# Performance work log

Measured on AMD Instinct MI355X. Metric: run time of the kernel, lower is better.

## Reference

```python
import jax, jax.numpy as jnp
import numpy as np

DIM = 768
TIME_DIM = 768
NUM_HEADS = 12
NUM_PATCHES = 784
GRID = 28  # sqrt(NUM_PATCHES)
REL_MAX = 2 * GRID - 1  # 55


def _rel_pos_indices():
    # Faithful to the torch buffer: relative_position_index = (dh + g-1) + (dw + g-1)
    coords = np.stack(np.meshgrid(np.arange(GRID), np.arange(GRID), indexing='ij'))  # [2,g,g]
    cf = coords.reshape(2, -1)  # [2,N]
    rel = cf[:, :, None] - cf[:, None, :]  # [2,N,N]
    rel = rel.transpose(1, 2, 0)
    rel[:, :, 0] += GRID - 1
    rel[:, :, 1] += GRID - 1
    idx = rel.sum(-1)  # [N,N], values in [0, 2*(2g-2)]
    # forward then splits this summed index (as written in the source):
    ih = idx // REL_MAX
    iw = idx % REL_MAX
    return jnp.asarray(ih, jnp.int32), jnp.asarray(iw, jnp.int32)


def setup_inputs() -> dict:
    key = jax.random.key(0)
    ks = jax.random.split(key, 16)
    B = 8
    s = 0.02
    inp = {
        'x_s': jax.random.normal(ks[0], (B, NUM_PATCHES, DIM), jnp.float32),
        'x_t': jax.random.normal(ks[1], (B, TIME_DIM), jnp.float32),
        'Wqs': jax.random.normal(ks[2], (DIM, DIM), jnp.float32) * s,
        'Wqt': jax.random.normal(ks[3], (TIME_DIM, DIM), jnp.float32) * s,
        'Wks': jax.random.normal(ks[4], (DIM, DIM), jnp.float32) * s,
        'Wkt': jax.random.normal(ks[5], (TIME_DIM, DIM), jnp.float32) * s,
        'Wvs': jax.random.normal(ks[6], (DIM, DIM), jnp.float32) * s,
        'Wvt': jax.random.normal(ks[7], (TIME_DIM, DIM), jnp.float32) * s,
        'rpb_table': jax.random.normal(ks[8], (REL_MAX, REL_MAX, NUM_HEADS), jnp.float32) * s,
        'proj_w': jax.random.normal(ks[9], (DIM, DIM), jnp.float32) * s,
        'proj_b': jnp.zeros((DIM,), jnp.float32),
    }
    return inp


def reference(x_s, x_t, Wqs, Wqt, Wks, Wkt, Wvs, Wvt, rpb_table, proj_w, proj_b):
    B, N, D = x_s.shape
    H = NUM_HEADS
    hd = D // H
    scale = hd ** -0.5

    # time-embed fused QKV: q = x_s @ Wqs + x_t @ Wqt (broadcast over tokens)
    q = x_s @ Wqs + (x_t @ Wqt)[:, None, :]
    k = x_s @ Wks + (x_t @ Wkt)[:, None, :]
    v = x_s @ Wvs + (x_t @ Wvt)[:, None, :]

    q = q.reshape(B, N, H, hd).transpose(0, 2, 1, 3)  # [B,H,N,hd]
    k = k.reshape(B, N, H, hd).transpose(0, 2, 1, 3)
    v = v.reshape(B, N, H, hd).transpose(0, 2, 1, 3)

    attn = jnp.einsum('bhnd,bhmd->bhnm', q, k) * scale  # [B,H,N,N]

    ih, iw = _rel_pos_indices()  # [N,N] each
    bias = rpb_table[ih, iw]  # [N,N,H]
    attn = attn + bias.transpose(2, 0, 1)[None]  # [1,H,N,N]

    attn = jax.nn.softmax(attn, axis=-1)
    x = jnp.einsum('bhnm,bhmd->bhnd', attn, v)
    x = x.transpose(0, 2, 1, 3).reshape(B, N, D)
    return x @ proj_w + proj_b
```

## Files before the change

kernel.cpp:

```cpp
#include <hip/hip_runtime.h>
#include <stdint.h>

#define DIM 768
#define NP  784
#define NH  12
#define HD  64
#define BATCH 8
#define MROWS (BATCH*NP)
#define MPAD 832
#define NCHUNK 32
#define KCH 24

using bf16x8 = __attribute__((ext_vector_type(8))) short;
using bf16x4 = __attribute__((ext_vector_type(4))) short;
using f32x4  = __attribute__((ext_vector_type(4))) float;

__device__ __forceinline__ short f2bf(float f) {
  union { float f; uint32_t u; } c; c.f = f;
  uint32_t u = c.u;
  u += 0x7FFFu + ((u >> 16) & 1u);
  return (short)(u >> 16);
}

__device__ __forceinline__ void gld_lds16(const void* g, void* l) {
  __builtin_amdgcn_global_load_lds((const __attribute__((address_space(1))) uint32_t*)g,
                                   (__attribute__((address_space(3))) uint32_t*)l,
                                   16, 0, 0);
}

__global__ __launch_bounds__(256) void cvt_bf16_kernel(const float* __restrict__ src,
                                                       short* __restrict__ dst, int n8) {
  int i = blockIdx.x * 256 + threadIdx.x;
  if (i >= n8) return;
  const float4* s = (const float4*)src;
  float4 a = s[2*i], b = s[2*i+1];
  bf16x8 o;
  o[0]=f2bf(a.x); o[1]=f2bf(a.y); o[2]=f2bf(a.z); o[3]=f2bf(a.w);
  o[4]=f2bf(b.x); o[5]=f2bf(b.y); o[6]=f2bf(b.z); o[7]=f2bf(b.w);
  ((bf16x8*)dst)[i] = o;
}

__global__ __launch_bounds__(256) void wtrans_kernel(const float* __restrict__ w0,
                                                     const float* __restrict__ w1,
                                                     const float* __restrict__ w2,
                                                     const float* __restrict__ w3,
                                                     short* __restrict__ dst) {
  __shared__ float tile[32][33];
  const int z = blockIdx.z;
  const float* src = (z==0) ? w0 : (z==1) ? w1 : (z==2) ? w2 : w3;
  short* d = dst + (size_t)z * DIM * DIM;
  const int n0 = blockIdx.x*32, k0 = blockIdx.y*32;
  const int tx = threadIdx.x, ty = threadIdx.y;
#pragma unroll
  for (int i=0;i<4;i++) tile[ty+i*8][tx] = src[(size_t)(k0+ty+i*8)*DIM + n0+tx];
  __syncthreads();
#pragma unroll
  for (int i=0;i<4;i++) d[(size_t)(n0+ty+i*8)*DIM + k0+tx] = f2bf(tile[tx][ty+i*8]);
}

__global__ __launch_bounds__(256) void tvec1_kernel(const float* __restrict__ x_t,
                                                    const float* __restrict__ wq,
                                                    const float* __restrict__ wk,
                                                    const float* __restrict__ wv,
                                                    float* __restrict__ part) {
  const int z = blockIdx.x, kc = blockIdx.y;
  const float* w = (z==0) ? wq : (z==1) ? wk : wv;
  const int d = threadIdx.x;
  __shared__ float xs[BATCH][KCH];
  if (threadIdx.x < BATCH*KCH)
    xs[threadIdx.x / KCH][threadIdx.x % KCH] =
        x_t[(size_t)(threadIdx.x / KCH)*DIM + kc*KCH + threadIdx.x % KCH];
  __syncthreads();
  float a0[BATCH] = {}, a1[BATCH] = {}, a2[BATCH] = {};
#pragma unroll 4
  for (int k = 0; k < KCH; ++k) {
    const float* wr = w + (size_t)(kc*KCH + k)*DIM + d;
    float w0 = wr[0], w1 = wr[256], w2 = wr[512];
#pragma unroll
    for (int b = 0; b < BATCH; ++b) {
      float xv = xs[b][k];
      a0[b] += xv*w0; a1[b] += xv*w1; a2[b] += xv*w2;
    }
  }
#pragma unroll
  for (int b = 0; b < BATCH; ++b) {
    float* p = part + (((size_t)z*NCHUNK + kc)*BATCH + b)*DIM + d;
    p[0] = a0[b]; p[256] = a1[b]; p[512] = a2[b];
  }
}

__global__ __launch_bounds__(256) void tvec2_kernel(const float* __restrict__ part,
                                                    float* __restrict__ t) {
  const int i = blockIdx.x*256 + threadIdx.x;
  if (i >= 3*BATCH*DIM) return;
  const int z = i / (BATCH*DIM), rem = i % (BATCH*DIM);
  float s = 0.f;
#pragma unroll 8
  for (int c = 0; c < NCHUNK; ++c)
    s += part[((size_t)z*NCHUNK + c)*BATCH*DIM + rem];
  t[i] = s;
}

template<int MODE>
__global__ __launch_bounds__(256) void gemm_kernel(const short* __restrict__ A,
                                                   const short* __restrict__ Bw,
                                                   const float* __restrict__ aux,
                                                   short* __restrict__ outq,
                                                   short* __restrict__ outk,
                                                   short* __restrict__ outv,
                                                   float* __restrict__ outf) {
  __shared__ short As[128*32];
  __shared__ short Bs[128*32];
  const int bx = blockIdx.x, by = blockIdx.y, z = blockIdx.z;
  const short* Bz = Bw + (size_t)z * DIM * DIM;
  const int tid = threadIdx.x, w = tid>>6, lane = tid&63;
  const int wr = w>>1, wc = w&1, ln15 = lane&15, lg = lane>>4;
  const int m0 = by*128, n0 = bx*128;

  f32x4 acc[4][4] = {};

  for (int kt=0; kt<24; ++kt) {
    const int k0 = kt*32;
    __syncthreads();
#pragma unroll
    for (int i=0;i<2;i++) {
      const int inst = w*2 + i;
      const int off  = inst*1024 + lane*16;
      const int row  = off >> 6;
      const int ce   = (off & 63) >> 1;
      gld_lds16(A  + (size_t)(m0+row)*DIM + k0 + ce, (char*)As + (size_t)inst*1024);
      gld_lds16(Bz + (size_t)(n0+row)*DIM + k0 + ce, (char*)Bs + (size_t)inst*1024);
    }
    __syncthreads();
    bf16x8 af[4], bfr[4];
#pragma unroll
    for (int mi=0;mi<4;mi++) af[mi]  = *(const bf16x8*)&As[(wr*64+mi*16+ln15)*32 + lg*8];
#pragma unroll
    for (int ni=0;ni<4;ni++) bfr[ni] = *(const bf16x8*)&Bs[(wc*64+ni*16+ln15)*32 + lg*8];
#pragma unroll
    for (int mi=0;mi<4;mi++)
#pragma unroll
      for (int ni=0;ni<4;ni++)
        acc[mi][ni] = __builtin_amdgcn_mfma_f32_16x16x32_bf16(af[mi], bfr[ni], acc[mi][ni], 0,0,0);
  }

  if (MODE == 0) {
    const float scl = (z==0) ? 0.125f : 1.0f;
#pragma unroll
    for (int mi=0;mi<4;mi++) {
#pragma unroll
      for (int j=0;j<4;j++) {
        const int r  = m0 + wr*64 + mi*16 + lg*4 + j;
        const int bb = r / NP;
        const int m  = r - bb*NP;
        const float* tv = aux + ((size_t)z*BATCH + bb) * DIM;
        if (z == 0) {
#pragma unroll
          for (int ni=0;ni<4;ni++) {
            const int gcol = n0 + wc*64 + ni*16 + ln15;
            outq[(size_t)r*DIM + gcol] = f2bf((acc[mi][ni][j] + tv[gcol]) * scl);
          }
        } else if (z == 1) {
#pragma unroll
          for (int ni=0;ni<4;ni++) {
            const int gcol = n0 + wc*64 + ni*16 + ln15;
            const int h = gcol >> 6, d = gcol & 63;
            outk[((size_t)(bb*NH + h)*MPAD + m)*HD + d] = f2bf(acc[mi][ni][j] + tv[gcol]);
          }
        }
      }
      if (MODE == 0 && z == 2) {
        const int r0 = m0 + wr*64 + mi*16 + lg*4;
        const int bb = r0 / NP;
        const int m  = r0 - bb*NP;
        const float* tv = aux + ((size_t)2*BATCH + bb) * DIM;
#pragma unroll
        for (int ni=0;ni<4;ni++) {
          const int gcol = n0 + wc*64 + ni*16 + ln15;
          const int h = gcol >> 6, d = gcol & 63;
          const float tb = tv[gcol];
          bf16x4 ov;
          ov[0] = f2bf(acc[mi][ni][0] + tb);
          ov[1] = f2bf(acc[mi][ni][1] + tb);
          ov[2] = f2bf(acc[mi][ni][2] + tb);
          ov[3] = f2bf(acc[mi][ni][3] + tb);
          *(bf16x4*)&outv[((size_t)(bb*NH + h)*HD + d)*MPAD + m] = ov;
        }
      }
    }
  } else {
#pragma unroll
    for (int mi=0;mi<4;mi++)
#pragma unroll
      for (int j=0;j<4;j++) {
        const int r = m0 + wr*64 + mi*16 + lg*4 + j;
#pragma unroll
        for (int ni=0;ni<4;ni++) {
          const int gcol = n0 + wc*64 + ni*16 + ln15;
          outf[(size_t)r*DIM + gcol] = acc[mi][ni][j] + aux[gcol];
        }
      }
  }
}

__global__ __launch_bounds__(256) void attn2_kernel(const short* __restrict__ Qb,
                                                    const short* __restrict__ Kt,
                                                    const short* __restrict__ Vt,
                                                    const float* __restrict__ rpb,
                                                    short* __restrict__ Ob) {
  __shared__ short kt[2][4096];
  __shared__ short vt[2][4096];
  __shared__ float bias_ext[112];
  __shared__ short msum[MPAD];
  const int qt = blockIdx.x, h = blockIdx.y, b = blockIdx.z;
  const int q0 = qt*64, tid = threadIdx.x, w = tid >> 6, lane = tid & 63;
  const int ln15 = lane & 15, lg = lane >> 4;

  if (tid < 109) bias_ext[tid + 2] = rpb[(tid/55)*(55*NH) + (tid%55)*NH + h];
  if (tid == 109) { bias_ext[0] = 0.f; bias_ext[1] = 0.f; bias_ext[111] = 0.f; }
  for (int i = tid; i < MPAD; i += 256) msum[i] = (short)(i/28 + i%28);

  const bool active = (q0 + w*16) < NP;
  const int q_idx = q0 + w*16 + ln15;
  bf16x8 qf0 = {}, qf1 = {};
  if (active) {
    const short* qp = Qb + ((size_t)(b*NP) + q_idx)*DIM + h*HD + lg*8;
    qf0 = *(const bf16x8*)qp;
    qf1 = *(const bf16x8*)(qp + 32);
  }
  const int qs = q_idx/28 + q_idx%28;

  const int lr = lane >> 3, lc = lane & 7;
  const int swe = (lc ^ lr) << 3;
  const size_t bh = (size_t)(b*NH + h);
  const short* kp0 = Kt + (bh*MPAD + (size_t)(w*8 + lr))*HD + swe;
  const short* kp1 = kp0 + 32*HD;
  const short* vp0 = Vt + (bh*HD + (size_t)(w*8 + lr))*MPAD + swe;
  const short* vp1 = vp0 + 32*MPAD;

#define STAGE4(BUF) { \
    char* kb_ = (char*)kt[BUF]; char* vb_ = (char*)vt[BUF]; \
    gld_lds16(kp0, kb_ + w*1024); \
    gld_lds16(kp1, kb_ + (w+4)*1024); \
    gld_lds16(vp0, vb_ + w*1024); \
    gld_lds16(vp1, vb_ + (w+4)*1024); \
    kp0 += 64*HD; kp1 += 64*HD; vp0 += 64; vp1 += 64; }

  float m_run = -3.0e38f, l_run = 0.f;
  f32x4 o0 = {}, o1 = {}, o2 = {}, o3 = {};

  STAGE4(0)

  for (int t = 0; t < 13; ++t) {
    const int cur = t & 1;
    const int m0 = t * 64;
    __syncthreads();
    if (t < 12) STAGE4(cur^1)
    if (active) {
      const char* kb = (const char*)kt[cur];
      const int sw = (ln15 & 7) << 4;
      f32x4 s[4];
#pragma unroll
      for (int mc = 0; mc < 4; ++mc) {
        const int rb = (mc*16 + ln15) * 128;
        bf16x8 kf0 = *(const bf16x8*)(kb + rb + ((lg*16) ^ sw));
        bf16x8 kf1 = *(const bf16x8*)(kb + rb + ((lg*16 + 64) ^ sw));
        f32x4 acc = {};
        acc = __builtin_amdgcn_mfma_f32_16x16x32_bf16(kf0, qf0, acc, 0,0,0);
        acc = __builtin_amdgcn_mfma_f32_16x16x32_bf16(kf1, qf1, acc, 0,0,0);
        s[mc] = acc;
      }
#pragma unroll
      for (int mc = 0; mc < 4; ++mc) {
        const int mb = m0 + mc*16 + lg*4;
        bf16x4 ms4 = *(const bf16x4*)&msum[mb];
#pragma unroll
        for (int j = 0; j < 4; ++j)
          s[mc][j] += bias_ext[qs - (int)ms4[j] + 56];
      }
      if (m0 + 64 > NP) {
#pragma unroll
        for (int mc = 0; mc < 4; ++mc)
#pragma unroll
          for (int j = 0; j < 4; ++j)
            if (m0 + mc*16 + lg*4 + j >= NP) s[mc][j] = -1e30f;
      }
      float tm = s[0][0];
#pragma unroll
      for (int mc = 0; mc < 4; ++mc)
#pragma unroll
        for (int j = 0; j < 4; ++j) tm = fmaxf(tm, s[mc][j]);
      tm = fmaxf(tm, __shfl_xor(tm, 16));
      tm = fmaxf(tm, __shfl_xor(tm, 32));
      const float m_new = fmaxf(m_run, tm);
      const float f = __expf(m_run - m_new);
      float ts = 0.f;
#pragma unroll
      for (int mc = 0; mc < 4; ++mc)
#pragma unroll
        for (int j = 0; j < 4; ++j) { float p = __expf(s[mc][j] - m_new); s[mc][j] = p; ts += p; }
      ts += __shfl_xor(ts, 16);
      ts += __shfl_xor(ts, 32);
      l_run = l_run * f + ts;
      m_run = m_new;
      o0 *= f; o1 *= f; o2 *= f; o3 *= f;
      bf16x4 pb[4];
#pragma unroll
      for (int mc = 0; mc < 4; ++mc) {
        pb[mc][0] = f2bf(s[mc][0]); pb[mc][1] = f2bf(s[mc][1]);
        pb[mc][2] = f2bf(s[mc][2]); pb[mc][3] = f2bf(s[mc][3]);
      }
      const char* vb = (const char*)vt[cur];
#pragma unroll
      for (int mc = 0; mc < 4; ++mc) {
        const int ib = (mc*32 + lg*8) ^ sw;
        bf16x4 vf0 = *(const bf16x4*)(vb + (0*16+ln15)*128 + ib);
        bf16x4 vf1 = *(const bf16x4*)(vb + (1*16+ln15)*128 + ib);
        bf16x4 vf2 = *(const bf16x4*)(vb + (2*16+ln15)*128 + ib);
        bf16x4 vf3 = *(const bf16x4*)(vb + (3*16+ln15)*128 + ib);
        o0 = __builtin_amdgcn_mfma_f32_16x16x16bf16_1k(vf0, pb[mc], o0, 0,0,0);
        o1 = __builtin_amdgcn_mfma_f32_16x16x16bf16_1k(vf1, pb[mc], o1, 0,0,0);
        o2 = __builtin_amdgcn_mfma_f32_16x16x16bf16_1k(vf2, pb[mc], o2, 0,0,0);
        o3 = __builtin_amdgcn_mfma_f32_16x16x16bf16_1k(vf3, pb[mc], o3, 0,0,0);
      }
    }
  }
#undef STAGE4

  if (active) {
    const float inv = 1.0f / l_run;
    short* op = Ob + ((size_t)(b*NP) + q_idx)*DIM + h*HD + lg*4;
    bf16x4 ov;
    ov[0]=f2bf(o0[0]*inv); ov[1]=f2bf(o0[1]*inv); ov[2]=f2bf(o0[2]*inv); ov[3]=f2bf(o0[3]*inv);
    *(bf16x4*)(op + 0*16) = ov;
    ov[0]=f2bf(o1[0]*inv); ov[1]=f2bf(o1[1]*inv); ov[2]=f2bf(o1[2]*inv); ov[3]=f2bf(o1[3]*inv);
    *(bf16x4*)(op + 1*16) = ov;
    ov[0]=f2bf(o2[0]*inv); ov[1]=f2bf(o2[1]*inv); ov[2]=f2bf(o2[2]*inv); ov[3]=f2bf(o2[3]*inv);
    *(bf16x4*)(op + 2*16) = ov;
    ov[0]=f2bf(o3[0]*inv); ov[1]=f2bf(o3[1]*inv); ov[2]=f2bf(o3[2]*inv); ov[3]=f2bf(o3[3]*inv);
    *(bf16x4*)(op + 3*16) = ov;
  }
}

extern "C" void kernel_launch(void* const* d_in, const int* in_sizes, int n_in,
                              void* d_out, int out_size, void* d_ws, size_t ws_size,
                              hipStream_t stream) {
  const float* x_s = (const float*)d_in[0];
  const float* x_t = (const float*)d_in[1];
  const float* Wqs = (const float*)d_in[2];
  const float* Wqt = (const float*)d_in[3];
  const float* Wks = (const float*)d_in[4];
  const float* Wkt = (const float*)d_in[5];
  const float* Wvs = (const float*)d_in[6];
  const float* Wvt = (const float*)d_in[7];
  const float* rpb = (const float*)d_in[8];
  const float* pw  = (const float*)d_in[9];
  const float* pb  = (const float*)d_in[10];
  float* out = (float*)d_out;

  char* ws = (char*)d_ws;
  size_t off = 0;
  float* t_part = (float*)(ws + off); off += (size_t)3*NCHUNK*BATCH*DIM*4;
  float* t_vec  = (float*)(ws + off); off += (size_t)3*BATCH*DIM*4;
  short* Wt     = (short*)(ws + off); off += (size_t)4*DIM*DIM*2;
  short* Qb     = (short*)(ws + off); off += (size_t)MROWS*DIM*2;
  short* Ob     = (short*)(ws + off); off += (size_t)MROWS*DIM*2;
  short* Xb     = (short*)(ws + off); off += (size_t)MROWS*DIM*2;
  short* Kt     = (short*)(ws + off); off += (size_t)BATCH*NH*MPAD*HD*2;
  short* Vt     = (short*)(ws + off); off += (size_t)BATCH*NH*MPAD*HD*2;

  cvt_bf16_kernel<<<2352, 256, 0, stream>>>(x_s, Xb, MROWS*DIM/8);
  wtrans_kernel<<<dim3(24,24,4), dim3(32,8), 0, stream>>>(Wqs, Wks, Wvs, pw, Wt);
  tvec1_kernel<<<dim3(3,NCHUNK), 256, 0, stream>>>(x_t, Wqt, Wkt, Wvt, t_part);
  tvec2_kernel<<<72, 256, 0, stream>>>(t_part, t_vec);
  gemm_kernel<0><<<dim3(6,49,3), 256, 0, stream>>>(Xb, Wt, t_vec, Qb, Kt, Vt, nullptr);
  attn2_kernel<<<dim3(13,NH,BATCH), 256, 0, stream>>>(Qb, Kt, Vt, rpb, Ob);
  gemm_kernel<1><<<dim3(6,49,1), 256, 0, stream>>>(Ob, Wt + (size_t)3*DIM*DIM, pb,
                                                   nullptr, nullptr, nullptr, out);
}
```

Baseline: 139.5 us.

## Use exp2 softmax with lazy rescale, arithmetic bias indexing, and XCD-aware block remap

Folds log2(e) into the Q scale and the bias table so the softmax can use exp2f directly. It skips the running-max rescale of the output accumulators unless the block max grows by more than 8, computes the relative-position bias index arithmetically instead of through a shared msum table, and converts with the hip bf16 intrinsic. The launch becomes a 1D grid remapped so consecutive blocks of one (batch, head) land on the same XCD for L2 reuse of K/V. The lazy rescale allows exp values up to 2^8 before renormalising, which may slightly change bf16 precision of P.

Result: no change. 139.4 us (-0.1%).

```diff
diff --git a/kernel.cpp b/kernel.cpp
--- a/kernel.cpp
+++ b/kernel.cpp
@@ -1,4 +1,5 @@
 #include <hip/hip_runtime.h>
+#include <hip/hip_bf16.h>
 #include <stdint.h>
 
 #define DIM 768
@@ -10,6 +11,7 @@
 #define MPAD 832
 #define NCHUNK 32
 #define KCH 24
+#define L2E 1.4426950408889634f
 
 using bf16x8 = __attribute__((ext_vector_type(8))) short;
 using bf16x4 = __attribute__((ext_vector_type(4))) short;
@@ -20,6 +22,12 @@
   uint32_t u = c.u;
   u += 0x7FFFu + ((u >> 16) & 1u);
   return (short)(u >> 16);
+}
+
+__device__ __forceinline__ short bfr(float x) {
+  union { __hip_bfloat16 b; short s; } u;
+  u.b = __float2bfloat16(x);
+  return u.s;
 }
 
 __device__ __forceinline__ void gld_lds16(const void* g, void* l) {
@@ -132,20 +140,20 @@
       gld_lds16(Bz + (size_t)(n0+row)*DIM + k0 + ce, (char*)Bs + (size_t)inst*1024);
     }
     __syncthreads();
-    bf16x8 af[4], bfr[4];
-#pragma unroll
-    for (int mi=0;mi<4;mi++) af[mi]  = *(const bf16x8*)&As[(wr*64+mi*16+ln15)*32 + lg*8];
-#pragma unroll
-    for (int ni=0;ni<4;ni++) bfr[ni] = *(const bf16x8*)&Bs[(wc*64+ni*16+ln15)*32 + lg*8];
+    bf16x8 af[4], bfr_[4];
+#pragma unroll
+    for (int mi=0;mi<4;mi++) af[mi]   = *(const bf16x8*)&As[(wr*64+mi*16+ln15)*32 + lg*8];
+#pragma unroll
+    for (int ni=0;ni<4;ni++) bfr_[ni] = *(const bf16x8*)&Bs[(wc*64+ni*16+ln15)*32 + lg*8];
 #pragma unroll
     for (int mi=0;mi<4;mi++)
 #pragma unroll
       for (int ni=0;ni<4;ni++)
-        acc[mi][ni] = __builtin_amdgcn_mfma_f32_16x16x32_bf16(af[mi], bfr[ni], acc[mi][ni], 0,0,0);
+        acc[mi][ni] = __builtin_amdgcn_mfma_f32_16x16x32_bf16(af[mi], bfr_[ni], acc[mi][ni], 0,0,0);
   }
 
   if (MODE == 0) {
-    const float scl = (z==0) ? 0.125f : 1.0f;
+    const float scl = (z==0) ? 0.125f * L2E : 1.0f;
 #pragma unroll
     for (int mi=0;mi<4;mi++) {
 #pragma unroll
@@ -203,7 +211,7 @@
   }
 }
 
-__global__ __launch_bounds__(256) void attn2_kernel(const short* __restrict__ Qb,
+__global__ __launch_bounds__(256) void attn3_kernel(const short* __restrict__ Qb,
                                                     const short* __restrict__ Kt,
                                                     const short* __restrict__ Vt,
                                                     const float* __restrict__ rpb,
@@ -211,14 +219,16 @@
   __shared__ short kt[2][4096];
   __shared__ short vt[2][4096];
   __shared__ float bias_ext[112];
-  __shared__ short msum[MPAD];
-  const int qt = blockIdx.x, h = blockIdx.y, b = blockIdx.z;
+  const int hw = blockIdx.x;
+  const int lgid = (hw & 7) * 156 + (hw >> 3);
+  const int qt = lgid % 13;
+  const int bh = lgid / 13;
+  const int h = bh % NH, b = bh / NH;
   const int q0 = qt*64, tid = threadIdx.x, w = tid >> 6, lane = tid & 63;
   const int ln15 = lane & 15, lg = lane >> 4;
 
-  if (tid < 109) bias_ext[tid + 2] = rpb[(tid/55)*(55*NH) + (tid%55)*NH + h];
+  if (tid < 109) bias_ext[tid + 2] = rpb[(tid/55)*(55*NH) + (tid%55)*NH + h] * L2E;
   if (tid == 109) { bias_ext[0] = 0.f; bias_ext[1] = 0.f; bias_ext[111] = 0.f; }
-  for (int i = tid; i < MPAD; i += 256) msum[i] = (short)(i/28 + i%28);
 
   const bool active = (q0 + w*16) < NP;
   const int q_idx = q0 + w*16 + ln15;
@@ -228,14 +238,14 @@
     qf0 = *(const bf16x8*)qp;
     qf1 = *(const bf16x8*)(qp + 32);
   }
-  const int qs = q_idx/28 + q_idx%28;
+  const int qs56 = q_idx/28 + q_idx%28 + 56;
 
   const int lr = lane >> 3, lc = lane & 7;
   const int swe = (lc ^ lr) << 3;
-  const size_t bh = (size_t)(b*NH + h);
-  const short* kp0 = Kt + (bh*MPAD + (size_t)(w*8 + lr))*HD + swe;
+  const size_t bhs = (size_t)bh;
+  const short* kp0 = Kt + (bhs*MPAD + (size_t)(w*8 + lr))*HD + swe;
   const short* kp1 = kp0 + 32*HD;
-  const short* vp0 = Vt + (bh*HD + (size_t)(w*8 + lr))*MPAD + swe;
+  const short* vp0 = Vt + (bhs*HD + (size_t)(w*8 + lr))*MPAD + swe;
   const short* vp1 = vp0 + 32*MPAD;
 
 #define STAGE4(BUF) { \
@@ -273,10 +283,12 @@
 #pragma unroll
       for (int mc = 0; mc < 4; ++mc) {
         const int mb = m0 + mc*16 + lg*4;
-        bf16x4 ms4 = *(const bf16x4*)&msum[mb];
-#pragma unroll
-        for (int j = 0; j < 4; ++j)
-          s[mc][j] += bias_ext[qs - (int)ms4[j] + 56];
+        const int a28 = (mb * 2341) >> 16;
+        const int idx0 = qs56 - mb + 27*a28;
+        s[mc][0] += bias_ext[idx0];
+        s[mc][1] += bias_ext[idx0-1];
+        s[mc][2] += bias_ext[idx0-2];
+        s[mc][3] += bias_ext[idx0-3];
       }
       if (m0 + 64 > NP) {
 #pragma unroll
@@ -285,30 +297,38 @@
           for (int j = 0; j < 4; ++j)
             if (m0 + mc*16 + lg*4 + j >= NP) s[mc][j] = -1e30f;
       }
-      float tm = s[0][0];
-#pragma unroll
-      for (int mc = 0; mc < 4; ++mc)
-#pragma unroll
-        for (int j = 0; j < 4; ++j) tm = fmaxf(tm, s[mc][j]);
+      float t0 = fmaxf(fmaxf(s[0][0],s[0][1]), fmaxf(s[0][2],s[0][3]));
+      float t1 = fmaxf(fmaxf(s[1][0],s[1][1]), fmaxf(s[1][2],s[1][3]));
+      float t2 = fmaxf(fmaxf(s[2][0],s[2][1]), fmaxf(s[2][2],s[2][3]));
+      float t3 = fmaxf(fmaxf(s[3][0],s[3][1]), fmaxf(s[3][2],s[3][3]));
+      float tm = fmaxf(fmaxf(t0,t1), fmaxf(t2,t3));
       tm = fmaxf(tm, __shfl_xor(tm, 16));
       tm = fmaxf(tm, __shfl_xor(tm, 32));
-      const float m_new = fmaxf(m_run, tm);
-      const float f = __expf(m_run - m_new);
+      const bool grow = !__all(tm - m_run <= 8.0f);
+      float m_new = m_run, f = 1.0f;
+      if (grow) { m_new = fmaxf(m_run, tm); f = exp2f(m_run - m_new); }
       float ts = 0.f;
 #pragma unroll
-      for (int mc = 0; mc < 4; ++mc)
-#pragma unroll
-        for (int j = 0; j < 4; ++j) { float p = __expf(s[mc][j] - m_new); s[mc][j] = p; ts += p; }
+      for (int mc = 0; mc < 4; ++mc) {
+        float p0 = exp2f(s[mc][0]-m_new), p1 = exp2f(s[mc][1]-m_new);
+        float p2 = exp2f(s[mc][2]-m_new), p3 = exp2f(s[mc][3]-m_new);
+        s[mc][0]=p0; s[mc][1]=p1; s[mc][2]=p2; s[mc][3]=p3;
+        ts += (p0+p1)+(p2+p3);
+      }
       ts += __shfl_xor(ts, 16);
       ts += __shfl_xor(ts, 32);
-      l_run = l_run * f + ts;
-      m_run = m_new;
-      o0 *= f; o1 *= f; o2 *= f; o3 *= f;
+      if (grow) {
+        l_run = l_run * f + ts;
+        m_run = m_new;
+        o0 *= f; o1 *= f; o2 *= f; o3 *= f;
+      } else {
+        l_run += ts;
+      }
       bf16x4 pb[4];
 #pragma unroll
       for (int mc = 0; mc < 4; ++mc) {
-        pb[mc][0] = f2bf(s[mc][0]); pb[mc][1] = f2bf(s[mc][1]);
-        pb[mc][2] = f2bf(s[mc][2]); pb[mc][3] = f2bf(s[mc][3]);
+        pb[mc][0] = bfr(s[mc][0]); pb[mc][1] = bfr(s[mc][1]);
+        pb[mc][2] = bfr(s[mc][2]); pb[mc][3] = bfr(s[mc][3]);
       }
       const char* vb = (const char*)vt[cur];
 #pragma unroll
@@ -331,13 +351,13 @@
     const float inv = 1.0f / l_run;
     short* op = Ob + ((size_t)(b*NP) + q_idx)*DIM + h*HD + lg*4;
     bf16x4 ov;
-    ov[0]=f2bf(o0[0]*inv); ov[1]=f2bf(o0[1]*inv); ov[2]=f2bf(o0[2]*inv); ov[3]=f2bf(o0[3]*inv);
+    ov[0]=bfr(o0[0]*inv); ov[1]=bfr(o0[1]*inv); ov[2]=bfr(o0[2]*inv); ov[3]=bfr(o0[3]*inv);
     *(bf16x4*)(op + 0*16) = ov;
-    ov[0]=f2bf(o1[0]*inv); ov[1]=f2bf(o1[1]*inv); ov[2]=f2bf(o1[2]*inv); ov[3]=f2bf(o1[3]*inv);
+    ov[0]=bfr(o1[0]*inv); ov[1]=bfr(o1[1]*inv); ov[2]=bfr(o1[2]*inv); ov[3]=bfr(o1[3]*inv);
     *(bf16x4*)(op + 1*16) = ov;
-    ov[0]=f2bf(o2[0]*inv); ov[1]=f2bf(o2[1]*inv); ov[2]=f2bf(o2[2]*inv); ov[3]=f2bf(o2[3]*inv);
+    ov[0]=bfr(o2[0]*inv); ov[1]=bfr(o2[1]*inv); ov[2]=bfr(o2[2]*inv); ov[3]=bfr(o2[3]*inv);
     *(bf16x4*)(op + 2*16) = ov;
-    ov[0]=f2bf(o3[0]*inv); ov[1]=f2bf(o3[1]*inv); ov[2]=f2bf(o3[2]*inv); ov[3]=f2bf(o3[3]*inv);
+    ov[0]=bfr(o3[0]*inv); ov[1]=bfr(o3[1]*inv); ov[2]=bfr(o3[2]*inv); ov[3]=bfr(o3[3]*inv);
     *(bf16x4*)(op + 3*16) = ov;
   }
 }
@@ -374,7 +394,7 @@
   tvec1_kernel<<<dim3(3,NCHUNK), 256, 0, stream>>>(x_t, Wqt, Wkt, Wvt, t_part);
   tvec2_kernel<<<72, 256, 0, stream>>>(t_part, t_vec);
   gemm_kernel<0><<<dim3(6,49,3), 256, 0, stream>>>(Xb, Wt, t_vec, Qb, Kt, Vt, nullptr);
-  attn2_kernel<<<dim3(13,NH,BATCH), 256, 0, stream>>>(Qb, Kt, Vt, rpb, Ob);
+  attn3_kernel<<<1248, 256, 0, stream>>>(Qb, Kt, Vt, rpb, Ob);
   gemm_kernel<1><<<dim3(6,49,1), 256, 0, stream>>>(Ob, Wt + (size_t)3*DIM*DIM, pb,
                                                    nullptr, nullptr, nullptr, out);
 }
```
